# Optimization experiments

Measured on AMD Instinct MI355X. Metric: run time of the kernel, lower is better.

## Reference

```python
import jax, jax.numpy as jnp
import numpy as np

DIM = 1024
H = 16
DH = DIM // H  # 64


def _l2norm(a):
    # matches torch F.normalize(dim=-1, eps=1e-12)
    n = jnp.linalg.norm(a, axis=-1, keepdims=True)
    return a / jnp.maximum(n, 1e-12)


def setup_inputs() -> dict:
    key = jax.random.key(0)
    ks = jax.random.split(key, 6)
    B, T = 4, 4096
    s = 0.02
    return {
        "x": jax.random.normal(ks[0], (B, T, DIM), jnp.float32),
        "Wqkv": jax.random.normal(ks[1], (3 * DIM, DIM), jnp.float32) * s,
        "Wg": jax.random.normal(ks[2], (H, DIM), jnp.float32) * s,
        "bg": jnp.zeros((H,), jnp.float32),
        "Wb": jax.random.normal(ks[3], (H, DIM), jnp.float32) * s,
        "bb": jnp.zeros((H,), jnp.float32),
        "Wout": jax.random.normal(ks[4], (DIM, DIM), jnp.float32) * s,
    }


def reference(x, Wqkv, Wg, bg, Wb, bb, Wout):
    B, T, D = x.shape
    qkv = (x @ Wqkv.T).reshape(B, T, 3, H, DH)
    q = _l2norm(qkv[:, :, 0])   # [B,T,H,Dh]
    k = _l2norm(qkv[:, :, 1])
    v = qkv[:, :, 2]
    alpha = jax.nn.sigmoid(x @ Wg.T + bg)  # [B,T,H]
    beta = jax.nn.sigmoid(x @ Wb.T + bb)   # [B,T,H]

    # time-major for scan
    qT = jnp.moveaxis(q, 1, 0)  # [T,B,H,Dh]
    kT = jnp.moveaxis(k, 1, 0)
    vT = jnp.moveaxis(v, 1, 0)
    aT = jnp.moveaxis(alpha, 1, 0)  # [T,B,H]
    bT = jnp.moveaxis(beta, 1, 0)

    S0 = jnp.zeros((B, H, DH, DH), jnp.float32)

    def step(S, inp):
        q_t, k_t, v_t, a_t, b_t = inp
        Sk = jnp.einsum('bhij,bhj->bhi', S, k_t)          # S @ k_t
        a = a_t[..., None, None]
        b = b_t[..., None, None]
        # S = a * (S - b * (S k) k^T) + b * v k^T
        S = a * (S - b * Sk[..., :, None] * k_t[..., None, :]) \
            + b * v_t[..., :, None] * k_t[..., None, :]
        o = jnp.einsum('bhij,bhj->bhi', S, q_t)
        return S, o

    _, outs = jax.lax.scan(step, S0, (qT, kT, vT, aT, bT))  # [T,B,H,Dh]
    out = jnp.moveaxis(outs, 0, 1).reshape(B, T, D)
    return out @ Wout.T
```

## Files before the change

kernel.cpp:

```cpp
#include <hip/hip_runtime.h>
#include <hip/hip_bf16.h>

#define NB   4
#define NT   4096
#define BT   16384
#define NDIM 1024
#define NH   16
#define NDH  64
#define CC   64
#define NCH  (NT / CC)
#define NPAIR 64
#define NU   (NPAIR * NCH)
#define DBS  24

using u16 = unsigned short;
typedef __bf16 bf16x8 __attribute__((ext_vector_type(8)));
typedef float f32x4 __attribute__((ext_vector_type(4)));
typedef unsigned short u16x8 __attribute__((ext_vector_type(8)));
typedef unsigned short u16x4 __attribute__((ext_vector_type(4)));

__device__ __forceinline__ float bf2f(u16 b) { return __uint_as_float(((unsigned)b) << 16); }
__device__ __forceinline__ u16 f2bf(float f) {
  return __builtin_bit_cast(u16, __float2bfloat16(f));
}
__device__ __forceinline__ int swz(int row, int e) { return e ^ ((row & 7) << 3); }
__device__ __forceinline__ bf16x8 zfrag() {
  u16x8 z = {0, 0, 0, 0, 0, 0, 0, 0};
  return __builtin_bit_cast(bf16x8, z);
}
__device__ __forceinline__ long qkvT_idx(int s, int h, long bt, int d) {
  return ((long)(s * 16 + h) * BT + bt) * 64 + d;
}

__global__ __launch_bounds__(256) void k_f32_to_bf16(const float* __restrict__ in,
                                                     u16* __restrict__ out, long n4) {
  long i = (long)blockIdx.x * blockDim.x + threadIdx.x;
  if (i >= n4) return;
  float4 f = reinterpret_cast<const float4*>(in)[i];
  u16x4 o;
  o.x = f2bf(f.x); o.y = f2bf(f.y); o.z = f2bf(f.z); o.w = f2bf(f.w);
  reinterpret_cast<u16x4*>(out)[i] = o;
}

__global__ __launch_bounds__(256) void k_build_wgb(const float* __restrict__ Wg,
                                                   const float* __restrict__ Wb,
                                                   u16* __restrict__ out) {
  int i = blockIdx.x * 256 + threadIdx.x;
  int row = i >> 10, col = i & 1023;
  float f = 0.f;
  if (row < 16)       f = Wg[row * 1024 + col];
  else if (row < 32)  f = Wb[(row - 16) * 1024 + col];
  out[i] = f2bf(f);
}

typedef unsigned int u32_as1 __attribute__((address_space(1)));
typedef unsigned int u32_as3 __attribute__((address_space(3)));
__device__ __forceinline__ void gload_lds16(const void* g, void* l) {
  __builtin_amdgcn_global_load_lds((const u32_as1*)g, (u32_as3*)l, 16, 0, 0);
}

template <typename OutT, bool QKVT>
__global__ __launch_bounds__(512, 2) void k_gemm256(const u16* __restrict__ A,
                                                    const u16* __restrict__ B,
                                                    OutT* __restrict__ C,
                                                    int M, int N, int K) {
  __shared__ __align__(16) u16 As[2][2][256 * 32];
  __shared__ __align__(16) u16 Bs[2][2][256 * 32];
  const int tid = threadIdx.x;
  const int l = tid & 63, w = tid >> 6;
  const int wm = w >> 2, wn = w & 3;
  const int fr = l & 15, fq = l >> 4;
  const int nwg = gridDim.x;
  const int cpx = nwg >> 3;
  const int bid = blockIdx.x;
  const int sbid = (bid & 7) * cpx + (bid >> 3);
  const int ntn = N >> 8;
  const int tm = sbid / ntn, tn = sbid - tm * ntn;
  const long a0 = (long)tm * 256 * K;
  const long b0 = (long)tn * 256 * K;
  const int srow0 = tid >> 2;
  const int scol8 = (((tid & 3) ^ ((tid >> 4) & 3)) << 3);
  const int cswz = ((fq ^ ((fr >> 2) & 3)) << 3);
  const int NKT = K >> 6;

  auto stage_half = [&](int kt, int buf, int hf) {
    const int ks = hf >> 1;
    const u16* Gp = (hf & 1) ? B : A;
    const long g0 = ((hf & 1) ? b0 : a0) + (long)kt * 64 + ks * 32 + scol8;
    u16* lb = (hf & 1) ? &Bs[buf][ks][w * 512] : &As[buf][ks][w * 512];
#pragma unroll
    for (int r = 0; r < 2; ++r)
      gload_lds16(Gp + g0 + (long)(r * 128 + srow0) * K, lb + r * 4096);
  };

  f32x4 acc[8][4];
#pragma unroll
  for (int m = 0; m < 8; ++m)
#pragma unroll
    for (int n = 0; n < 4; ++n) acc[m][n] = f32x4{0.f, 0.f, 0.f, 0.f};

  auto domfma = [&](f32x4& a, const bf16x8& af, const bf16x8& bf_) {
    if constexpr (QKVT) a = __builtin_amdgcn_mfma_f32_16x16x32_bf16(bf_, af, a, 0, 0, 0);
    else                a = __builtin_amdgcn_mfma_f32_16x16x32_bf16(af, bf_, a, 0, 0, 0);
  };

  stage_half(0, 0, 0); stage_half(0, 0, 1); stage_half(0, 0, 2); stage_half(0, 0, 3);

  for (int kt = 0; kt < NKT; ++kt) {
    const int bi = kt & 1;
    const bool pf = (kt + 1 < NKT);
    asm volatile("s_waitcnt vmcnt(4)" ::: "memory");
    __builtin_amdgcn_sched_barrier(0);
    __builtin_amdgcn_s_barrier();
    __builtin_amdgcn_sched_barrier(0);
    {
      const u16* ap = &As[bi][0][(wm * 128 + fr) * 32 + cswz];
      const u16* bp = &Bs[bi][0][(wn * 64 + fr) * 32 + cswz];
      bf16x8 bfr[4], afr[4];
#pragma unroll
      for (int n = 0; n < 4; ++n) bfr[n] = *(const bf16x8*)(bp + n * 512);
#pragma unroll
      for (int m = 0; m < 4; ++m) afr[m] = *(const bf16x8*)(ap + m * 512);
      if (pf) stage_half(kt + 1, bi ^ 1, 0);
      __builtin_amdgcn_s_setprio(1);
#pragma unroll
      for (int m = 0; m < 4; ++m)
#pragma unroll
        for (int n = 0; n < 4; ++n) domfma(acc[m][n], afr[m], bfr[n]);
      __builtin_amdgcn_s_setprio(0);
#pragma unroll
      for (int m = 0; m < 4; ++m) afr[m] = *(const bf16x8*)(ap + (4 + m) * 512);
      if (pf) stage_half(kt + 1, bi ^ 1, 1);
      __builtin_amdgcn_s_setprio(1);
#pragma unroll
      for (int m = 0; m < 4; ++m)
#pragma unroll
        for (int n = 0; n < 4; ++n) domfma(acc[4 + m][n], afr[m], bfr[n]);
      __builtin_amdgcn_s_setprio(0);
    }
    if (pf) { asm volatile("s_waitcnt vmcnt(4)" ::: "memory"); }
    else    { asm volatile("s_waitcnt vmcnt(0)" ::: "memory"); }
    __builtin_amdgcn_sched_barrier(0);
    __builtin_amdgcn_s_barrier();
    __builtin_amdgcn_sched_barrier(0);
    {
      const u16* ap = &As[bi][1][(wm * 128 + fr) * 32 + cswz];
      const u16* bp = &Bs[bi][1][(wn * 64 + fr) * 32 + cswz];
      bf16x8 bfr[4], afr[4];
#pragma unroll
      for (int n = 0; n < 4; ++n) bfr[n] = *(const bf16x8*)(bp + n * 512);
#pragma unroll
      for (int m = 0; m < 4; ++m) afr[m] = *(const bf16x8*)(ap + m * 512);
      if (pf) stage_half(kt + 1, bi ^ 1, 2);
      __builtin_amdgcn_s_setprio(1);
#pragma unroll
      for (int m = 0; m < 4; ++m)
#pragma unroll
        for (int n = 0; n < 4; ++n) domfma(acc[m][n], afr[m], bfr[n]);
      __builtin_amdgcn_s_setprio(0);
#pragma unroll
      for (int m = 0; m < 4; ++m) afr[m] = *(const bf16x8*)(ap + (4 + m) * 512);
      if (pf) stage_half(kt + 1, bi ^ 1, 3);
      __builtin_amdgcn_s_setprio(1);
#pragma unroll
      for (int m = 0; m < 4; ++m)
#pragma unroll
        for (int n = 0; n < 4; ++n) domfma(acc[4 + m][n], afr[m], bfr[n]);
      __builtin_amdgcn_s_setprio(0);
    }
  }

  if constexpr (QKVT) {
    const int hb = (tn * 256 + wn * 64) >> 6;
#pragma unroll
    for (int m = 0; m < 8; ++m) {
      const long bt = (long)tm * 256 + wm * 128 + m * 16 + fr;
#pragma unroll
      for (int n = 0; n < 4; ++n) {
        u16x4 o;
#pragma unroll
        for (int r = 0; r < 4; ++r) o[r] = f2bf(acc[m][n][r]);
        *(u16x4*)&C[((long)hb * BT + bt) * 64 + n * 16 + fq * 4] = o;
      }
    }
  } else {
#pragma unroll
    for (int m = 0; m < 8; ++m)
#pragma unroll
      for (int n = 0; n < 4; ++n) {
        const int row0 = tm * 256 + wm * 128 + m * 16 + fq * 4;
        const int col  = tn * 256 + wn * 64 + n * 16 + fr;
#pragma unroll
        for (int r = 0; r < 4; ++r) {
          long idx = (long)(row0 + r) * N + col;
          if constexpr (sizeof(OutT) == 2) C[idx] = f2bf(acc[m][n][r]);
          else                             C[idx] = acc[m][n][r];
        }
      }
  }
}

__global__ __launch_bounds__(256) void k_gates(const u16* __restrict__ xb,
                                               const u16* __restrict__ wgb,
                                               const float* __restrict__ bg,
                                               const float* __restrict__ bb,
                                               float* __restrict__ alpha,
                                               float* __restrict__ beta) {
  __shared__ __align__(16) u16 As[128 * 64];
  __shared__ __align__(16) u16 Bs[32 * 64];
  const int tid = threadIdx.x, l = tid & 63, w = tid >> 6;
  const int fr = l & 15, fq = l >> 4;
  const int tm = blockIdx.x;
  const long a0 = (long)tm * 128 * 1024;

  f32x4 acc[2][2];
#pragma unroll
  for (int m = 0; m < 2; ++m)
#pragma unroll
    for (int n = 0; n < 2; ++n) acc[m][n] = f32x4{0.f, 0.f, 0.f, 0.f};

  for (int kk = 0; kk < 1024; kk += 64) {
    __syncthreads();
#pragma unroll
    for (int p = 0; p < 4; ++p) {
      const int idx = p * 256 + tid;
      const int row = idx >> 3;
      const int c8 = ((idx & 7) ^ (row & 7)) << 3;
      gload_lds16(&xb[a0 + (long)row * 1024 + kk + c8], &As[p * 2048 + w * 512]);
    }
    {
      const int row = tid >> 3;
      const int c8 = ((tid & 7) ^ (row & 7)) << 3;
      gload_lds16(&wgb[(long)row * 1024 + kk + c8], &Bs[w * 512]);
    }
    asm volatile("s_waitcnt vmcnt(0)" ::: "memory");
    __syncthreads();
#pragma unroll
    for (int ks = 0; ks < 2; ++ks) {
      bf16x8 af[2], bfv[2];
#pragma unroll
      for (int m = 0; m < 2; ++m) {
        const int row = w * 32 + m * 16 + fr;
        af[m] = __builtin_bit_cast(bf16x8, *(const u16x8*)&As[row * 64 + swz(row, ks * 32 + fq * 8)]);
      }
#pragma unroll
      for (int n = 0; n < 2; ++n) {
        const int row = n * 16 + fr;
        bfv[n] = __builtin_bit_cast(bf16x8, *(const u16x8*)&Bs[row * 64 + swz(row, ks * 32 + fq * 8)]);
      }
#pragma unroll
      for (int m = 0; m < 2; ++m)
#pragma unroll
        for (int n = 0; n < 2; ++n)
          acc[m][n] = __builtin_amdgcn_mfma_f32_16x16x32_bf16(af[m], bfv[n], acc[m][n], 0, 0, 0);
    }
  }
  const float bgv = bg[fr], bbv = bb[fr];
#pragma unroll
  for (int m = 0; m < 2; ++m)
#pragma unroll
    for (int r = 0; r < 4; ++r) {
      const long row = (long)tm * 128 + w * 32 + m * 16 + fq * 4 + r;
      alpha[row * 16 + fr] = 1.f / (1.f + __expf(-(acc[m][0][r] + bgv)));
      beta[row * 16 + fr]  = 1.f / (1.f + __expf(-(acc[m][1][r] + bbv)));
    }
}

__global__ __launch_bounds__(256, 3) void k_prep(u16* __restrict__ qkv,
                                                 const float* __restrict__ alpha,
                                                 const float* __restrict__ beta,
                                                 float* __restrict__ A63G,
                                                 u16* __restrict__ oi) {
  __shared__ __align__(16) u16 Ks[64 * 64];
  __shared__ __align__(16) u16 WTs[128 * 64];
  __shared__ __align__(16) u16 Lb[64 * 64];
  __shared__ __align__(16) u16 MqS[64 * 64];
  __shared__ __align__(16) u16 KdT[64 * 64];
  __shared__ __align__(16) u16 Db[4 * 16 * DBS];
  __shared__ float cvec[64], Avec[64], Ainvv[64], bvec[64], nkinv[64], nqinv[64];

  const int unit = blockIdx.x;
  const int pair = unit >> 6, ch = unit & 63;
  const int b = pair >> 4, h = pair & 15;
  const int tid = threadIdx.x, l = tid & 63, w = tid >> 6;
  const int fr = l & 15, fq = l >> 4;
  const long t0 = (long)b * NT + (long)ch * CC;

  u16x8 kreg[2], vreg[2], qreg[2];
  int srow_[2], sseg_[2];
#pragma unroll
  for (int p = 0; p < 2; ++p) {
    int idx = p * 256 + tid;
    srow_[p] = idx >> 3; sseg_[p] = (idx & 7) * 8;
    qreg[p] = *(const u16x8*)&qkv[qkvT_idx(0, h, t0 + srow_[p], sseg_[p])];
    kreg[p] = *(const u16x8*)&qkv[qkvT_idx(1, h, t0 + srow_[p], sseg_[p])];
    vreg[p] = *(const u16x8*)&qkv[qkvT_idx(2, h, t0 + srow_[p], sseg_[p])];
  }
  const int ar = w * 16 + fr;
  u16x8 qa[2];
#pragma unroll
  for (int kk = 0; kk < 2; ++kk)
    qa[kk] = *(const u16x8*)&qkv[qkvT_idx(0, h, t0 + ar, kk * 32 + fq * 8)];

  if (w == 0) {
    float av = alpha[(t0 + l) * 16 + h];
    float bv = beta[(t0 + l) * 16 + h];
    float cl = __log2f(av);
#pragma unroll
    for (int d = 1; d < 64; d <<= 1) {
      float up = __shfl_up(cl, d);
      if (l >= d) cl += up;
    }
    float A = exp2f(cl);
    cvec[l] = cl; Avec[l] = A; Ainvv[l] = exp2f(-cl); bvec[l] = bv;
    if (l == 63) A63G[unit] = A;
  }
  __syncthreads();

#pragma unroll
  for (int p = 0; p < 2; ++p) {
    int row = srow_[p], seg = sseg_[p];
    *(u16x8*)&Ks[row * 64 + swz(row, seg)] = kreg[p];
    float kss = 0.f, qss = 0.f;
    const float bs = bvec[row];
#pragma unroll
    for (int e = 0; e < 8; ++e) {
      float kf = bf2f(kreg[p][e]), qf = bf2f(qreg[p][e]);
      kss += kf * kf; qss += qf * qf;
      int c = seg + e;
      WTs[c * 64 + swz(c, row)] = f2bf(bs * bf2f(vreg[p][e]));
    }
    kss += __shfl_xor(kss, 1); kss += __shfl_xor(kss, 2); kss += __shfl_xor(kss, 4);
    qss += __shfl_xor(qss, 1); qss += __shfl_xor(qss, 2); qss += __shfl_xor(qss, 4);
    if ((tid & 7) == 0) { nkinv[row] = kss; nqinv[row] = qss; }
  }
  __syncthreads();

  if (tid < 64)       nkinv[tid] = rsqrtf(fmaxf(nkinv[tid], 1e-24f));
  else if (tid < 128) nqinv[tid - 64] = rsqrtf(fmaxf(nqinv[tid - 64], 1e-24f));
  __syncthreads();

  f32x4 akk[4], aqk[4];
#pragma unroll
  for (int n = 0; n < 4; ++n) { akk[n] = f32x4{0, 0, 0, 0}; aqk[n] = f32x4{0, 0, 0, 0}; }
  {
    bf16x8 afK[2], afQ[2];
#pragma unroll
    for (int kk = 0; kk < 2; ++kk) {
      afK[kk] = __builtin_bit_cast(bf16x8, *(const u16x8*)&Ks[ar * 64 + swz(ar, kk * 32 + fq * 8)]);
      afQ[kk] = __builtin_bit_cast(bf16x8, qa[kk]);
    }
#pragma unroll
    for (int n = 0; n < 4; ++n) {
      const int br = n * 16 + fr;
#pragma unroll
      for (int kk = 0; kk < 2; ++kk) {
        bf16x8 bk = __builtin_bit_cast(bf16x8, *(const u16x8*)&Ks[br * 64 + swz(br, kk * 32 + fq * 8)]);
        akk[n] = __builtin_amdgcn_mfma_f32_16x16x32_bf16(afK[kk], bk, akk[n], 0, 0, 0);
        aqk[n] = __builtin_amdgcn_mfma_f32_16x16x32_bf16(afQ[kk], bk, aqk[n], 0, 0, 0);
      }
    }
  }
  {
    const int j = tid & 63, tg4 = tid >> 6;
    const float A63v = Avec[63];
    u16 kb[16], kd[16];
#pragma unroll
    for (int tt = 0; tt < 16; ++tt) {
      int t = tg4 * 16 + tt;
      float kv = bf2f(Ks[t * 64 + swz(t, j)]) * nkinv[t];
      kb[tt] = f2bf(bvec[t] * Avec[t] * kv);
      kd[tt] = f2bf(A63v * Ainvv[t] * kv);
    }
#pragma unroll
    for (int g8 = 0; g8 < 2; ++g8) {
      u16x8 o1, o2;
#pragma unroll
      for (int e = 0; e < 8; ++e) { o1[e] = kb[g8 * 8 + e]; o2[e] = kd[g8 * 8 + e]; }
      int colg = tg4 * 16 + g8 * 8;
      *(u16x8*)&WTs[(64 + j) * 64 + swz(64 + j, colg)] = o1;
      *(u16x8*)&KdT[j * 64 + swz(j, colg)] = o2;
    }
  }
#pragma unroll
  for (int n = 0; n < 4; ++n)
#pragma unroll
    for (int r = 0; r < 4; ++r) {
      const int t = w * 16 + fq * 4 + r;
      const int s = n * 16 + fr;
      const float e = Avec[t] * Ainvv[s];
      Lb[t * 64 + swz(t, s)] = (s < t) ? f2bf(bvec[t] * e * nkinv[t] * nkinv[s] * akk[n][r]) : (u16)0;
      MqS[t * 64 + swz(t, s)] = (s <= t) ? f2bf(e * nqinv[t] * nkinv[s] * aqk[n][r]) : (u16)0;
    }
  __syncthreads();

  if (l < 16) {
    const int c = l;
    const int rb = w * 16;
    float x[16];
#pragma unroll
    for (int u = 0; u < 16; ++u) {
      float a2 = (u == c) ? 1.f : 0.f;
#pragma unroll
      for (int s = 0; s < u; ++s)
        a2 -= bf2f(Lb[(rb + u) * 64 + swz(rb + u, rb + s)]) * x[s];
      x[u] = a2;
    }
#pragma unroll
    for (int u = 0; u < 16; ++u)
      Db[w * 16 * DBS + u * DBS + c] = f2bf(x[u]);
  }
  __syncthreads();

  float ltil[6];
  {
    const int pbi[6] = {1, 2, 2, 3, 3, 3}, pbj[6] = {0, 0, 1, 0, 1, 2};
    const int tt = tid >> 4, s = tid & 15;
#pragma unroll
    for (int e = 0; e < 6; ++e) {
      int bi = pbi[e], bj = pbj[e];
      float a2 = 0.f;
#pragma unroll
      for (int u = 0; u < 16; ++u)
        a2 += bf2f(Db[bi * 16 * DBS + tt * DBS + u]) *
              bf2f(Lb[(bi * 16 + u) * 64 + swz(bi * 16 + u, bj * 16 + s)]);
      ltil[e] = a2;
    }
  }
  f32x4 rtacc[2][4];
#pragma unroll
  for (int rt2 = 0; rt2 < 2; ++rt2) {
    const int rrow = (w * 2 + rt2) * 16 + fr;
#pragma unroll
    for (int bi = 0; bi < 4; ++bi) {
      bf16x8 a2 = (fq < 2)
        ? __builtin_bit_cast(bf16x8, *(const u16x8*)&WTs[rrow * 64 + swz(rrow, bi * 16 + fq * 8)])
        : zfrag();
      bf16x8 b2 = (fq < 2)
        ? __builtin_bit_cast(bf16x8, *(const u16x8*)&Db[bi * 16 * DBS + fr * DBS + fq * 8])
        : zfrag();
      rtacc[rt2][bi] = __builtin_amdgcn_mfma_f32_16x16x32_bf16(a2, b2, f32x4{0, 0, 0, 0}, 0, 0, 0);
    }
  }
  __syncthreads();
  {
    const int pbi[6] = {1, 2, 2, 3, 3, 3}, pbj[6] = {0, 0, 1, 0, 1, 2};
    const int tt = tid >> 4, s = tid & 15;
#pragma unroll
    for (int e = 0; e < 6; ++e)
      Lb[(pbi[e] * 16 + tt) * 64 + swz(pbi[e] * 16 + tt, pbj[e] * 16 + s)] = f2bf(-ltil[e]);
  }
#pragma unroll
  for (int rt2 = 0; rt2 < 2; ++rt2)
#pragma unroll
    for (int bi = 0; bi < 4; ++bi)
#pragma unroll
      for (int r = 0; r < 4; ++r) {
        int rr = (w * 2 + rt2) * 16 + fq * 4 + r;
        WTs[rr * 64 + swz(rr, bi * 16 + fr)] = f2bf(rtacc[rt2][bi][r]);
      }
  __syncthreads();

#pragma unroll
  for (int rt2 = 0; rt2 < 2; ++rt2) {
    const int rrow = (w * 2 + rt2) * 16 + fr;
    const int wr0 = (w * 2 + rt2) * 16 + fq * 4;
#pragma unroll
    for (int i = 1; i < 4; ++i) {
      f32x4 a2;
#pragma unroll
      for (int r = 0; r < 4; ++r)
        a2[r] = bf2f(WTs[(wr0 + r) * 64 + swz(wr0 + r, i * 16 + fr)]);
      {
        bf16x8 af = __builtin_bit_cast(bf16x8, *(const u16x8*)&WTs[rrow * 64 + swz(rrow, fq * 8)]);
        bf16x8 bf_;
        if (i == 1) bf_ = (fq < 2)
          ? __builtin_bit_cast(bf16x8, *(const u16x8*)&Lb[(16 + fr) * 64 + swz(16 + fr, fq * 8)])
          : zfrag();
        else bf_ = __builtin_bit_cast(bf16x8, *(const u16x8*)&Lb[(i * 16 + fr) * 64 + swz(i * 16 + fr, fq * 8)]);
        a2 = __builtin_amdgcn_mfma_f32_16x16x32_bf16(af, bf_, a2, 0, 0, 0);
      }
      if (i == 3) {
        bf16x8 af = __builtin_bit_cast(bf16x8, *(const u16x8*)&WTs[rrow * 64 + swz(rrow, 32 + fq * 8)]);
        bf16x8 bf_ = (fq < 2)
          ? __builtin_bit_cast(bf16x8, *(const u16x8*)&Lb[(48 + fr) * 64 + swz(48 + fr, 32 + fq * 8)])
          : zfrag();
        a2 = __builtin_amdgcn_mfma_f32_16x16x32_bf16(af, bf_, a2, 0, 0, 0);
      }
#pragma unroll
      for (int r = 0; r < 4; ++r)
        WTs[(wr0 + r) * 64 + swz(wr0 + r, i * 16 + fr)] = f2bf(a2[r]);
    }
  }
  __syncthreads();

  const int prow = w * 16 + fr;
  u16x4 qpre4[4];
#pragma unroll
  for (int n = 0; n < 4; ++n)
    qpre4[n] = *(const u16x4*)&qkv[qkvT_idx(0, h, t0 + prow, n * 16 + fq * 4)];

  f32x4 aG[4], aU[4], aQe[4], aOi[4];
#pragma unroll
  for (int n = 0; n < 4; ++n) {
    aG[n] = f32x4{0, 0, 0, 0}; aU[n] = f32x4{0, 0, 0, 0};
    aQe[n] = f32x4{0, 0, 0, 0}; aOi[n] = f32x4{0, 0, 0, 0};
  }
  {
    bf16x8 aKd[2], aWv[2], aMq[2];
#pragma unroll
    for (int kk = 0; kk < 2; ++kk) {
      aKd[kk] = __builtin_bit_cast(bf16x8, *(const u16x8*)&KdT[ar * 64 + swz(ar, kk * 32 + fq * 8)]);
      aWv[kk] = __builtin_bit_cast(bf16x8, *(const u16x8*)&WTs[ar * 64 + swz(ar, kk * 32 + fq * 8)]);
      aMq[kk] = __builtin_bit_cast(bf16x8, *(const u16x8*)&MqS[ar * 64 + swz(ar, kk * 32 + fq * 8)]);
    }
#pragma unroll
    for (int n = 0; n < 4; ++n) {
      const int br = n * 16 + fr;
#pragma unroll
      for (int kk = 0; kk < 2; ++kk) {
        bf16x8 bTw = __builtin_bit_cast(bf16x8, *(const u16x8*)&WTs[(64 + br) * 64 + swz(64 + br, kk * 32 + fq * 8)]);
        bf16x8 bKd = __builtin_bit_cast(bf16x8, *(const u16x8*)&KdT[br * 64 + swz(br, kk * 32 + fq * 8)]);
        bf16x8 bWv = __builtin_bit_cast(bf16x8, *(const u16x8*)&WTs[br * 64 + swz(br, kk * 32 + fq * 8)]);
        aG[n]  = __builtin_amdgcn_mfma_f32_16x16x32_bf16(bTw, aKd[kk], aG[n], 0, 0, 0);
        aU[n]  = __builtin_amdgcn_mfma_f32_16x16x32_bf16(bKd, aWv[kk], aU[n], 0, 0, 0);
        aQe[n] = __builtin_amdgcn_mfma_f32_16x16x32_bf16(bTw, aMq[kk], aQe[n], 0, 0, 0);
        aOi[n] = __builtin_amdgcn_mfma_f32_16x16x32_bf16(bWv, aMq[kk], aOi[n], 0, 0, 0);
      }
    }
  }
  asm volatile("s_waitcnt vmcnt(0)" ::: "memory");
  __builtin_amdgcn_sched_barrier(0);
  const float aqs = Avec[prow] * nqinv[prow];
#pragma unroll
  for (int n = 0; n < 4; ++n) {
    u16x4 vq, vg, vu, vo;
#pragma unroll
    for (int r = 0; r < 4; ++r) {
      vq[r] = f2bf(aqs * bf2f(qpre4[n][r]) - aQe[n][r]);
      vg[r] = f2bf(-aG[n][r]);
      vu[r] = f2bf(aU[n][r]);
      vo[r] = f2bf(aOi[n][r]);
    }
    const int scol = swz(prow, n * 16 + fq * 4);
    *(u16x4*)&qkv[qkvT_idx(0, h, t0 + prow, scol)] = vq;
    *(u16x4*)&qkv[qkvT_idx(1, h, t0 + prow, scol)] = vg;
    *(u16x4*)&qkv[qkvT_idx(2, h, t0 + prow, scol)] = vu;
    *(u16x4*)&Ks[prow * 64 + scol] = vo;
  }
  __syncthreads();
#pragma unroll
  for (int p = 0; p < 2; ++p) {
    const int idx = p * 256 + tid;
    const int row = idx >> 3, seg = (idx & 7) * 8;
    *(u16x8*)&oi[(long)unit * 4096 + row * 64 + seg] = *(const u16x8*)&Ks[row * 64 + swz(row, seg)];
  }
}

__global__ __launch_bounds__(1024) void k_seq(const u16* __restrict__ qkv,
                                              const u16* __restrict__ oi,
                                              const float* __restrict__ A63G,
                                              u16* __restrict__ ob) {
  __shared__ __align__(16) u16 Sb[2][64 * 64];
  __shared__ __align__(16) u16 Obs[2][64 * 64];
  __shared__ __align__(16) u16 stg[3][4][64 * 64];
  __shared__ float a63s[64];
  const int pair = blockIdx.x;
  const int b = pair >> 4, h = pair & 15;
  const int tid = threadIdx.x, l = tid & 63, w = tid >> 6;
  const int fr = l & 15, fq = l >> 4;
  const int tw = w >> 2, td = w & 3;

  auto stage = [&](int c) {
    const int s = c % 3;
    const long tg = (long)b * NT + (long)c * CC;
    if (tid < 512) {
      const int row = tid >> 3, seg = (tid & 7) * 8;
#pragma unroll
      for (int m = 0; m < 4; ++m) {
        const u16* src = (m < 3)
          ? &qkv[qkvT_idx(m, h, tg + row, seg)]
          : &oi[(long)(pair * 64 + c) * 4096 + row * 64 + seg];
        gload_lds16(src, &stg[s][m][row * 64 + seg]);
      }
    }
  };

  if (tid < 64) a63s[tid] = A63G[pair * 64 + tid];
  for (int i = tid; i < 4096; i += 1024) Sb[0][i] = 0;
  stage(0); stage(1);
  f32x4 sacc = f32x4{0, 0, 0, 0};
  asm volatile("s_waitcnt lgkmcnt(0)" ::: "memory");
  __builtin_amdgcn_sched_barrier(0);

  for (int c = 0; c < NCH; ++c) {
    const int sb = c & 1, st = c % 3;
    const long tg = (long)b * NT + (long)c * CC;
    if (c <= 1)             { asm volatile("s_waitcnt vmcnt(4)" ::: "memory"); }
    else if (c < NCH - 1)   { asm volatile("s_waitcnt vmcnt(5)" ::: "memory"); }
    else                    { asm volatile("s_waitcnt vmcnt(1)" ::: "memory"); }
    __builtin_amdgcn_sched_barrier(0);
    __builtin_amdgcn_s_barrier();
    __builtin_amdgcn_sched_barrier(0);

    if (c > 0 && tid < 512) {
      const int row = tid >> 3, seg = (tid & 7) * 8;
      *(u16x8*)&ob[(tg - CC + row) * 1024 + h * 64 + seg] = *(const u16x8*)&Obs[sb ^ 1][row * 64 + seg];
    }
    if (c + 2 < NCH) stage(c + 2);

    const u16* Qe = stg[st][0];
    const u16* Gm = stg[st][1];
    const u16* Um = stg[st][2];
    const u16* Obl = stg[st][3];

    const int at = tw * 16 + fr;
    const int bd = td * 16 + fr;
    f32x4 ao = f32x4{0, 0, 0, 0};
    const float A63 = a63s[c];
#pragma unroll
    for (int r = 0; r < 4; ++r) sacc[r] *= A63;
#pragma unroll
    for (int kk = 0; kk < 2; ++kk) {
      bf16x8 aq = __builtin_bit_cast(bf16x8, *(const u16x8*)&Qe[at * 64 + swz(at, kk * 32 + fq * 8)]);
      bf16x8 sbf = __builtin_bit_cast(bf16x8, *(const u16x8*)&Sb[sb][bd * 64 + swz(bd, kk * 32 + fq * 8)]);
      ao = __builtin_amdgcn_mfma_f32_16x16x32_bf16(aq, sbf, ao, 0, 0, 0);
      bf16x8 as_ = __builtin_bit_cast(bf16x8, *(const u16x8*)&Sb[sb][at * 64 + swz(at, kk * 32 + fq * 8)]);
      bf16x8 g  = __builtin_bit_cast(bf16x8, *(const u16x8*)&Gm[bd * 64 + swz(bd, kk * 32 + fq * 8)]);
      sacc = __builtin_amdgcn_mfma_f32_16x16x32_bf16(as_, g, sacc, 0, 0, 0);
    }
#pragma unroll
    for (int r = 0; r < 4; ++r) {
      const int ri = tw * 16 + fq * 4 + r;
      const int cj = td * 16 + fr;
      sacc[r] += bf2f(Um[ri * 64 + swz(ri, cj)]);
      Obs[sb][ri * 64 + cj] = f2bf(bf2f(Obl[ri * 64 + cj]) + ao[r]);
      Sb[sb ^ 1][ri * 64 + swz(ri, cj)] = f2bf(sacc[r]);
    }
    asm volatile("s_waitcnt lgkmcnt(0)" ::: "memory");
    __builtin_amdgcn_sched_barrier(0);
  }
  __builtin_amdgcn_s_barrier();
  if (tid < 512) {
    const int row = tid >> 3, seg = (tid & 7) * 8;
    const long tg = (long)b * NT + (long)(NCH - 1) * CC;
    *(u16x8*)&ob[(tg + row) * 1024 + h * 64 + seg] = *(const u16x8*)&Obs[(NCH - 1) & 1][row * 64 + seg];
  }
}

extern "C" void kernel_launch(void* const* d_in, const int* in_sizes, int n_in,
                              void* d_out, int out_size, void* d_ws, size_t ws_size,
                              hipStream_t stream) {
  const float* x    = (const float*)d_in[0];
  const float* Wqkv = (const float*)d_in[1];
  const float* Wg   = (const float*)d_in[2];
  const float* bg   = (const float*)d_in[3];
  const float* Wb   = (const float*)d_in[4];
  const float* bb   = (const float*)d_in[5];
  const float* Wout = (const float*)d_in[6];
  float* out = (float*)d_out;

  char* ws = (char*)d_ws;
  u16* xb    = (u16*)ws;
  u16* wqkvb = xb    + (long)BT * NDIM;
  u16* woutb = wqkvb + (long)3072 * 1024;
  u16* wgbb  = woutb + (long)1024 * 1024;
  u16* qkvb  = wgbb  + (long)128 * 1024;
  u16* ob    = qkvb  + (long)BT * 3072;
  float* graw  = (float*)(ob + (long)BT * NDIM);
  float* alpha = graw + (long)BT * 128;
  float* beta  = alpha + (long)BT * NH;
  float* A63G  = graw;
  u16*   oi    = xb;

  k_f32_to_bf16<<<(BT * (long)NDIM / 4 + 255) / 256, 256, 0, stream>>>(x, xb, BT * (long)NDIM / 4);
  k_f32_to_bf16<<<(3072L * 1024 / 4 + 255) / 256, 256, 0, stream>>>(Wqkv, wqkvb, 3072L * 1024 / 4);
  k_f32_to_bf16<<<(1024L * 1024 / 4 + 255) / 256, 256, 0, stream>>>(Wout, woutb, 1024L * 1024 / 4);
  k_build_wgb<<<(128 * 1024) / 256, 256, 0, stream>>>(Wg, Wb, wgbb);

  k_gemm256<u16, true><<<64 * 12, 512, 0, stream>>>(xb, wqkvb, qkvb, BT, 3072, NDIM);

  k_gates<<<BT / 128, 256, 0, stream>>>(xb, wgbb, bg, bb, alpha, beta);

  k_prep<<<NU, 256, 0, stream>>>(qkvb, alpha, beta, A63G, oi);
  k_seq<<<NPAIR, 1024, 0, stream>>>(qkvb, oi, A63G, ob);

  k_gemm256<float, false><<<64 * 4, 512, 0, stream>>>(ob, woutb, out, BT, NDIM, NDIM);
}
```

Before: 362.0 us.

## Use four-slot ring buffer with three-stage prefetch in GEMM K loop

Replaces the double-buffered GEMM mainloop (two K-halves per buffer) with a 4-slot ring of 32-wide K slices, prefetching three slices ahead and waiting with vmcnt(8). The goal is to hide more global-to-LDS latency behind the MFMA work. Shared memory use stays the same. The deeper prefetch keeps more loads in flight, and the vmcnt accounting and slot reuse must stay exactly right to avoid races.

```diff
diff --git a/kernel.cpp b/kernel.cpp
--- a/kernel.cpp
+++ b/kernel.cpp
@@ -64,8 +64,8 @@
                                                     const u16* __restrict__ B,
                                                     OutT* __restrict__ C,
                                                     int M, int N, int K) {
-  __shared__ __align__(16) u16 As[2][2][256 * 32];
-  __shared__ __align__(16) u16 Bs[2][2][256 * 32];
+  __shared__ __align__(16) u16 As[4][256 * 32];
+  __shared__ __align__(16) u16 Bs[4][256 * 32];
   const int tid = threadIdx.x;
   const int l = tid & 63, w = tid >> 6;
   const int wm = w >> 2, wn = w & 3;
@@ -82,12 +82,14 @@
   const int scol8 = (((tid & 3) ^ ((tid >> 4) & 3)) << 3);
   const int cswz = ((fq ^ ((fr >> 2) & 3)) << 3);
   const int NKT = K >> 6;
-
-  auto stage_half = [&](int kt, int buf, int hf) {
-    const int ks = hf >> 1;
-    const u16* Gp = (hf & 1) ? B : A;
-    const long g0 = ((hf & 1) ? b0 : a0) + (long)kt * 64 + ks * 32 + scol8;
-    u16* lb = (hf & 1) ? &Bs[buf][ks][w * 512] : &As[buf][ks][w * 512];
+  const int NHALF = NKT * 2;
+
+  auto stage_part = [&](int j, int part) {
+    const int slot = j & 3;
+    const int kt = j >> 1, ks = j & 1;
+    const u16* Gp = part ? B : A;
+    const long g0 = (part ? b0 : a0) + (long)kt * 64 + ks * 32 + scol8;
+    u16* lb = part ? &Bs[slot][w * 512] : &As[slot][w * 512];
 #pragma unroll
     for (int r = 0; r < 2; ++r)
       gload_lds16(Gp + g0 + (long)(r * 128 + srow0) * K, lb + r * 4096);
@@ -104,70 +106,42 @@
     else                a = __builtin_amdgcn_mfma_f32_16x16x32_bf16(af, bf_, a, 0, 0, 0);
   };
 
-  stage_half(0, 0, 0); stage_half(0, 0, 1); stage_half(0, 0, 2); stage_half(0, 0, 3);
-
-  for (int kt = 0; kt < NKT; ++kt) {
-    const int bi = kt & 1;
-    const bool pf = (kt + 1 < NKT);
-    asm volatile("s_waitcnt vmcnt(4)" ::: "memory");
+  stage_part(0, 0); stage_part(0, 1);
+  stage_part(1, 0); stage_part(1, 1);
+  stage_part(2, 0); stage_part(2, 1);
+
+  for (int j = 0; j < NHALF; ++j) {
+    const int slot = j & 3;
+    if (j + 2 < NHALF)      { asm volatile("s_waitcnt vmcnt(8)" ::: "memory"); }
+    else if (j + 1 < NHALF) { asm volatile("s_waitcnt vmcnt(4)" ::: "memory"); }
+    else                    { asm volatile("s_waitcnt vmcnt(0)" ::: "memory"); }
     __builtin_amdgcn_sched_barrier(0);
     __builtin_amdgcn_s_barrier();
     __builtin_amdgcn_sched_barrier(0);
-    {
-      const u16* ap = &As[bi][0][(wm * 128 + fr) * 32 + cswz];
-      const u16* bp = &Bs[bi][0][(wn * 64 + fr) * 32 + cswz];
-      bf16x8 bfr[4], afr[4];
-#pragma unroll
-      for (int n = 0; n < 4; ++n) bfr[n] = *(const bf16x8*)(bp + n * 512);
-#pragma unroll
-      for (int m = 0; m < 4; ++m) afr[m] = *(const bf16x8*)(ap + m * 512);
-      if (pf) stage_half(kt + 1, bi ^ 1, 0);
-      __builtin_amdgcn_s_setprio(1);
-#pragma unroll
-      for (int m = 0; m < 4; ++m)
-#pragma unroll
-        for (int n = 0; n < 4; ++n) domfma(acc[m][n], afr[m], bfr[n]);
-      __builtin_amdgcn_s_setprio(0);
-#pragma unroll
-      for (int m = 0; m < 4; ++m) afr[m] = *(const bf16x8*)(ap + (4 + m) * 512);
-      if (pf) stage_half(kt + 1, bi ^ 1, 1);
-      __builtin_amdgcn_s_setprio(1);
-#pragma unroll
-      for (int m = 0; m < 4; ++m)
-#pragma unroll
-        for (int n = 0; n < 4; ++n) domfma(acc[4 + m][n], afr[m], bfr[n]);
-      __builtin_amdgcn_s_setprio(0);
-    }
-    if (pf) { asm volatile("s_waitcnt vmcnt(4)" ::: "memory"); }
-    else    { asm volatile("s_waitcnt vmcnt(0)" ::: "memory"); }
-    __builtin_amdgcn_sched_barrier(0);
-    __builtin_amdgcn_s_barrier();
-    __builtin_amdgcn_sched_barrier(0);
-    {
-      const u16* ap = &As[bi][1][(wm * 128 + fr) * 32 + cswz];
-      const u16* bp = &Bs[bi][1][(wn * 64 + fr) * 32 + cswz];
-      bf16x8 bfr[4], afr[4];
-#pragma unroll
-      for (int n = 0; n < 4; ++n) bfr[n] = *(const bf16x8*)(bp + n * 512);
-#pragma unroll
-      for (int m = 0; m < 4; ++m) afr[m] = *(const bf16x8*)(ap + m * 512);
-      if (pf) stage_half(kt + 1, bi ^ 1, 2);
-      __builtin_amdgcn_s_setprio(1);
-#pragma unroll
-      for (int m = 0; m < 4; ++m)
-#pragma unroll
-        for (int n = 0; n < 4; ++n) domfma(acc[m][n], afr[m], bfr[n]);
-      __builtin_amdgcn_s_setprio(0);
-#pragma unroll
-      for (int m = 0; m < 4; ++m) afr[m] = *(const bf16x8*)(ap + (4 + m) * 512);
-      if (pf) stage_half(kt + 1, bi ^ 1, 3);
-      __builtin_amdgcn_s_setprio(1);
-#pragma unroll
-      for (int m = 0; m < 4; ++m)
-#pragma unroll
-        for (int n = 0; n < 4; ++n) domfma(acc[4 + m][n], afr[m], bfr[n]);
-      __builtin_amdgcn_s_setprio(0);
-    }
+
+    const u16* ap = &As[slot][(wm * 128 + fr) * 32 + cswz];
+    const u16* bp = &Bs[slot][(wn * 64 + fr) * 32 + cswz];
+    bf16x8 bfr[4], afr[4];
+#pragma unroll
+    for (int n = 0; n < 4; ++n) bfr[n] = *(const bf16x8*)(bp + n * 512);
+#pragma unroll
+    for (int m = 0; m < 4; ++m) afr[m] = *(const bf16x8*)(ap + m * 512);
+    if (j + 3 < NHALF) stage_part(j + 3, 0);
+    __builtin_amdgcn_s_setprio(1);
+#pragma unroll
+    for (int m = 0; m < 4; ++m)
+#pragma unroll
+      for (int n = 0; n < 4; ++n) domfma(acc[m][n], afr[m], bfr[n]);
+    __builtin_amdgcn_s_setprio(0);
+#pragma unroll
+    for (int m = 0; m < 4; ++m) afr[m] = *(const bf16x8*)(ap + (4 + m) * 512);
+    if (j + 3 < NHALF) stage_part(j + 3, 1);
+    __builtin_amdgcn_s_setprio(1);
+#pragma unroll
+    for (int m = 0; m < 4; ++m)
+#pragma unroll
+      for (int n = 0; n < 4; ++n) domfma(acc[4 + m][n], afr[m], bfr[n]);
+    __builtin_amdgcn_s_setprio(0);
   }
 
   if constexpr (QKVT) {
```

Result: no change. 360.0 us, median of 2 (-0.6%).
